# Kernel tuning notes

Measured on AMD Instinct MI355X. Metric: run time of the kernel, lower is better.

## Reference

```python
import jax, jax.numpy as jnp
import numpy as np

N_NODES = 100000
N_EDGES = 1600000
F_IN = 512
D_EMB = 128
D_HID = 64
N_CLS = 32
EPS = 1e-5


def setup_inputs() -> dict:
    key = jax.random.key(0)
    ks = jax.random.split(key, 16)
    def w(k, shape):
        fan_in = shape[0]
        return jax.random.normal(k, shape, dtype=jnp.float32) / jnp.sqrt(jnp.float32(fan_in))
    return {
        "x": jax.random.normal(ks[0], (N_NODES, F_IN), dtype=jnp.float32),
        "W1": w(ks[1], (F_IN, D_EMB)), "b1": jnp.zeros((D_EMB,), jnp.float32),
        "Wc1": w(ks[2], (D_EMB, D_HID)), "bc1": jnp.zeros((D_HID,), jnp.float32),
        "Wc2": w(ks[3], (D_HID, D_HID)), "bc2": jnp.zeros((D_HID,), jnp.float32),
        "Wc3": w(ks[4], (D_HID, D_HID)), "bc3": jnp.zeros((D_HID,), jnp.float32),
        "gamma": jnp.ones((D_HID,), jnp.float32), "beta": jnp.zeros((D_HID,), jnp.float32),
        "W2": w(ks[5], (D_HID, N_CLS)), "b2": jnp.zeros((N_CLS,), jnp.float32),
        "W3": w(ks[6], (N_CLS, N_CLS)), "b3": jnp.zeros((N_CLS,), jnp.float32),
        "edge_index": jax.random.randint(ks[7], (2, N_EDGES), 0, N_NODES, dtype=jnp.int32),
    }


def _agg_mean(h, src, dst, n):
    # gather source-node features along edges, sum into destination nodes, divide by degree
    s = jax.ops.segment_sum(h[src], dst, num_segments=n)          # [N, d]
    deg = jax.ops.segment_sum(jnp.ones((src.shape[0], 1), h.dtype), dst, num_segments=n)
    return s / jnp.maximum(deg, 1.0)


def _conv1p(h, src, dst, W, b):
    # ConvolutionalLayer_1P: neighborhood gather/aggregate -> linear -> relu
    return jax.nn.relu(_agg_mean(h, src, dst, h.shape[0]) @ W + b)


def reference(x, W1, b1, Wc1, bc1, Wc2, bc2, Wc3, bc3, gamma, beta, W2, b2, W3, b3, edge_index):
    src, dst = edge_index[0], edge_index[1]
    # linmaps1 on 0th-order ptensors == identity copy
    h = jax.nn.relu(x @ W1 + b1)                 # lin1 + relu (dropout = identity in eval)
    h = _conv1p(h, src, dst, Wc1, bc1)           # conv1
    h = _conv1p(h, src, dst, Wc2, bc2)           # conv2
    h = _conv1p(h, src, dst, Wc3, bc3)           # conv3
    mean = jnp.mean(h, axis=0)
    var = jnp.var(h, axis=0)
    h = (h - mean) * jax.lax.rsqrt(var + EPS) * gamma + beta  # batchnorm (batch stats)
    h = jax.nn.relu(h @ W2 + b2)                 # lin2 + relu (dropout = identity)
    out = h @ W3 + b3                            # lin3; linmaps0 == identity
    return out
```

## Files before the change

kernel.cpp:

```cpp
#include <hip/hip_runtime.h>
#include <cstdint>
#include <cstddef>

constexpr int F_IN  = 512;
constexpr int D_EMB = 128;
constexpr int D_HID = 64;
constexpr int N_CLS = 32;

typedef __attribute__((ext_vector_type(8))) short short8;
typedef __attribute__((ext_vector_type(4))) float floatx4;

__device__ inline unsigned short f2bf(float f) {
  union { float f; uint32_t u; } v; v.f = f;
  uint32_t r = v.u + 0x7FFF + ((v.u >> 16) & 1);
  return (unsigned short)(r >> 16);
}

__global__ __launch_bounds__(256) void wt_kernel(
    const float* __restrict__ W1, short8* __restrict__ Wt2)
{
  int idx = blockIdx.x * 256 + threadIdx.x;
  int kc8 = idx >> 10, lin = idx & 1023;
  int ct = lin >> 7, rem = lin & 127, ks = rem >> 6, ln = rem & 63;
  int col = ct * 16 + (ln & 15);
  int k0 = kc8 * 64 + ks * 32 + (ln >> 4) * 8;
  short8 s;
#pragma unroll
  for (int j = 0; j < 8; ++j)
    s[j] = (short)f2bf(W1[(size_t)(k0 + j) * D_EMB + col]);
  Wt2[idx] = s;
}

__global__ __launch_bounds__(256) void lin1_mfma_kernel(
    const float* __restrict__ X, const short8* __restrict__ Wt2,
    const float* __restrict__ b1, float* __restrict__ H1, int n)
{
  __shared__ short8 Ws[1024];
  __shared__ short8 Xs[1024];

  const int t = threadIdx.x;
  const int wave = t >> 6, lane = t & 63;
  const int quad = lane >> 4, mrow = lane & 15;
  const int node0 = blockIdx.x * 128;
  const int rloc = (wave >> 1) * 64;
  const int cw = (wave & 1) * 4;

  const float* sp[4];
  int soff[4];
#pragma unroll
  for (int i = 0; i < 4; ++i) {
    int g = t + i * 256;
    int row = g >> 3, col8 = g & 7;
    soff[i] = row * 128 + ((col8 * 16) ^ ((row & 7) << 4));
    int gr = node0 + row; if (gr >= n) gr = n - 1;
    sp[i] = &X[(size_t)gr * F_IN + col8 * 8];
  }

  floatx4 acc[4][4];
#pragma unroll
  for (int i = 0; i < 4; ++i)
#pragma unroll
    for (int j = 0; j < 4; ++j) acc[i][j] = (floatx4){0.f, 0.f, 0.f, 0.f};

  float4 xr[4][2];
  short8 wr[4];

#pragma unroll
  for (int i = 0; i < 4; ++i) {
    const float* p = sp[i];
    xr[i][0] = *(const float4*)p;
    xr[i][1] = *(const float4*)(p + 4);
    wr[i] = Wt2[t + i * 256];
  }

  for (int kc8 = 0; kc8 < 8; ++kc8) {
    short8 s8[4];
#pragma unroll
    for (int i = 0; i < 4; ++i) {
      s8[i][0] = (short)f2bf(xr[i][0].x); s8[i][1] = (short)f2bf(xr[i][0].y);
      s8[i][2] = (short)f2bf(xr[i][0].z); s8[i][3] = (short)f2bf(xr[i][0].w);
      s8[i][4] = (short)f2bf(xr[i][1].x); s8[i][5] = (short)f2bf(xr[i][1].y);
      s8[i][6] = (short)f2bf(xr[i][1].z); s8[i][7] = (short)f2bf(xr[i][1].w);
    }
    __syncthreads();
#pragma unroll
    for (int i = 0; i < 4; ++i) {
      *(short8*)((char*)Xs + soff[i]) = s8[i];
      Ws[t + i * 256] = wr[i];
    }
    __syncthreads();

    if (kc8 < 7) {
#pragma unroll
      for (int i = 0; i < 4; ++i) {
        const float* p = sp[i] + (kc8 + 1) * 64;
        xr[i][0] = *(const float4*)p;
        xr[i][1] = *(const float4*)(p + 4);
        wr[i] = Wt2[(kc8 + 1) * 1024 + t + i * 256];
      }
    }

#pragma unroll
    for (int ks = 0; ks < 2; ++ks) {
      short8 af[4], bf[4];
#pragma unroll
      for (int rt = 0; rt < 4; ++rt) {
        int row = rloc + rt * 16 + mrow;
        int byteoff = row * 128 + ((ks * 64 + quad * 16) ^ ((row & 7) << 4));
        af[rt] = *(const short8*)((const char*)Xs + byteoff);
      }
#pragma unroll
      for (int c = 0; c < 4; ++c)
        bf[c] = Ws[((cw + c) * 2 + ks) * 64 + lane];
#pragma unroll
      for (int rt = 0; rt < 4; ++rt)
#pragma unroll
        for (int c = 0; c < 4; ++c)
          acc[rt][c] = __builtin_amdgcn_mfma_f32_16x16x32_bf16(
              af[rt], bf[c], acc[rt][c], 0, 0, 0);
    }
  }

  const int rowbase = node0 + rloc;
#pragma unroll
  for (int ct = 0; ct < 4; ++ct) {
    int col = (cw + ct) * 16 + mrow;
    float bias = b1[col];
#pragma unroll
    for (int rt = 0; rt < 4; ++rt) {
#pragma unroll
      for (int r = 0; r < 4; ++r) {
        int gn = rowbase + rt * 16 + quad * 4 + r;
        if (gn < n)
          H1[(size_t)gn * D_EMB + col] = fmaxf(acc[rt][ct][r] + bias, 0.f);
      }
    }
  }
}

template<int K, bool PRE>
__global__ __launch_bounds__(256) void mm_kernel(
    const float* __restrict__ In, const int* __restrict__ deg,
    const float* __restrict__ bin, const float* __restrict__ W,
    float* __restrict__ Out, int n)
{
  __shared__ float Hs[64][K + 4];
  __shared__ float Ws[K][64];
  const int t = threadIdx.x;
  const int node0 = blockIdx.x * 64;
  constexpr int KQ = K / 4;

#pragma unroll
  for (int i = 0; i < (64 * KQ) / 256; ++i) {
    int lin = t + i * 256;
    int node = lin / KQ, kq = lin % KQ;
    int gn = node0 + node;
    float4 v = make_float4(0.f, 0.f, 0.f, 0.f);
    if (gn < n) {
      v = *(const float4*)&In[(size_t)gn * K + kq * 4];
      if (PRE) {
        float rd = 1.f / fmaxf((float)deg[gn], 1.f);
        v.x = fmaxf(v.x * rd + bin[kq * 4 + 0], 0.f);
        v.y = fmaxf(v.y * rd + bin[kq * 4 + 1], 0.f);
        v.z = fmaxf(v.z * rd + bin[kq * 4 + 2], 0.f);
        v.w = fmaxf(v.w * rd + bin[kq * 4 + 3], 0.f);
      }
    }
    *(float4*)&Hs[node][kq * 4] = v;
  }
#pragma unroll
  for (int i = 0; i < (K * 64) / 1024; ++i) {
    int lin = t + i * 256;
    ((float4*)&Ws[0][0])[lin] = ((const float4*)W)[lin];
  }
  __syncthreads();

  const int rg = t >> 4, cg = t & 15;
  float acc[4][4];
#pragma unroll
  for (int i = 0; i < 4; ++i)
#pragma unroll
    for (int j = 0; j < 4; ++j) acc[i][j] = 0.f;

#pragma unroll 8
  for (int k = 0; k < K; ++k) {
    float a[4] = {Hs[rg*4+0][k], Hs[rg*4+1][k], Hs[rg*4+2][k], Hs[rg*4+3][k]};
    float4 b = *(const float4*)&Ws[k][cg * 4];
#pragma unroll
    for (int i = 0; i < 4; ++i) {
      acc[i][0] += a[i]*b.x; acc[i][1] += a[i]*b.y;
      acc[i][2] += a[i]*b.z; acc[i][3] += a[i]*b.w;
    }
  }
#pragma unroll
  for (int i = 0; i < 4; ++i) {
    int gn = node0 + rg * 4 + i;
    if (gn < n) {
      float4 o = make_float4(acc[i][0], acc[i][1], acc[i][2], acc[i][3]);
      *(float4*)&Out[(size_t)gn * 64 + cg * 4] = o;
    }
  }
}


__global__ __launch_bounds__(256) void hist_kernel(
    const int* __restrict__ dst, int* __restrict__ G, int nE, int B, int NB)
{
  __shared__ int h[256];
  int blk = blockIdx.x, t = threadIdx.x;
  h[t] = 0;
  __syncthreads();
  int base = blk * 8192;
  int lim = min(8192, nE - base);
  for (int i = t; i < lim; i += 256)
    atomicAdd(&h[dst[base + i] >> 9], 1);
  __syncthreads();
  if (t < NB) G[t * B + blk] = h[t];
}

__global__ __launch_bounds__(256) void scan1_kernel(
    const int* __restrict__ in, int* __restrict__ out,
    int* __restrict__ bsum, int n)
{
  __shared__ int sh[256];
  int t = threadIdx.x;
  int i = blockIdx.x * 256 + t;
  int c = (i < n) ? in[i] : 0;
  sh[t] = c;
  __syncthreads();
#pragma unroll
  for (int off = 1; off < 256; off <<= 1) {
    int v = 0;
    if (t >= off) v = sh[t - off];
    __syncthreads();
    if (t >= off) sh[t] += v;
    __syncthreads();
  }
  if (i < n) out[i] = sh[t] - c;
  if (t == 255) bsum[blockIdx.x] = sh[255];
}

__global__ __launch_bounds__(256) void scan2_kernel(int* __restrict__ bsum, int nb)
{
  __shared__ int sh[256];
  __shared__ int carry;
  int t = threadIdx.x;
  if (t == 0) carry = 0;
  __syncthreads();
  for (int base = 0; base < nb; base += 256) {
    int i = base + t;
    int v = (i < nb) ? bsum[i] : 0;
    sh[t] = v;
    __syncthreads();
#pragma unroll
    for (int off = 1; off < 256; off <<= 1) {
      int u = 0;
      if (t >= off) u = sh[t - off];
      __syncthreads();
      if (t >= off) sh[t] += u;
      __syncthreads();
    }
    int c0 = carry;
    int incl = sh[t], total = sh[255];
    if (i < nb) bsum[i] = c0 + incl - v;
    __syncthreads();
    if (t == 0) carry = c0 + total;
    __syncthreads();
  }
  if (t == 0) bsum[nb] = carry;
}

__global__ __launch_bounds__(256) void scan3_kernel(
    int* __restrict__ W, const int* __restrict__ bsum, int NG, int nb)
{
  int i = blockIdx.x * 256 + threadIdx.x;
  if (i < NG) W[i] += bsum[i >> 8];
  else if (i == NG) W[NG] = bsum[nb];
}

__global__ __launch_bounds__(256) void scatter2_kernel(
    const int* __restrict__ src, const int* __restrict__ dst,
    const int* __restrict__ W, int2* __restrict__ EP, int nE, int B, int NB)
{
  __shared__ int cur[256];
  int blk = blockIdx.x, t = threadIdx.x;
  if (t < NB) cur[t] = W[t * B + blk];
  __syncthreads();
  int base = blk * 8192;
  int lim = min(8192, nE - base);
  for (int i = t; i < lim; i += 256) {
    int s = src[base + i], d = dst[base + i];
    int slot = atomicAdd(&cur[d >> 9], 1);
    EP[slot] = make_int2(s, d);
  }
}

__global__ __launch_bounds__(256) void fillc_kernel(
    const int2* __restrict__ EP, const int* __restrict__ W,
    int* __restrict__ cnt, int* __restrict__ offs, int* __restrict__ adj,
    int n, int nE, int B, int NB)
{
  __shared__ int h[512];
  int b = blockIdx.x, t = threadIdx.x;
  int segStart = W[b * B];
  int segEnd = (b == NB - 1) ? nE : W[(b + 1) * B];
  int nodeBase = b << 9;

  h[t] = 0; h[t + 256] = 0;
  __syncthreads();
  for (int i = segStart + t; i < segEnd; i += 256)
    atomicAdd(&h[EP[i].y - nodeBase], 1);
  __syncthreads();
  int c0 = h[t], c1 = h[t + 256];
#pragma unroll
  for (int off = 1; off < 512; off <<= 1) {
    int a = (t >= off) ? h[t - off] : 0;
    int bb = (t + 256 >= off) ? h[t + 256 - off] : 0;
    __syncthreads();
    h[t] += a; h[t + 256] += bb;
    __syncthreads();
  }
  int e0 = h[t] - c0, e1 = h[t + 256] - c1;
  int g0 = nodeBase + t, g1 = nodeBase + t + 256;
  if (g0 < n) { cnt[g0] = c0; offs[g0] = segStart + e0; }
  if (g1 < n) { cnt[g1] = c1; offs[g1] = segStart + e1; }
  if (b == 0 && t == 0) offs[n] = nE;
  __syncthreads();
  h[t] = e0; h[t + 256] = e1;
  __syncthreads();
  for (int i = segStart + t; i < segEnd; i += 256) {
    int2 p = EP[i];
    int slot = atomicAdd(&h[p.y - nodeBase], 1);
    adj[segStart + slot] = p.x;
  }
}

__global__ __launch_bounds__(256) void gather_kernel(
    const float* __restrict__ P, const int* __restrict__ offs,
    const int* __restrict__ adj, float* __restrict__ A, int n)
{
  int node = (blockIdx.x * 256 + threadIdx.x) >> 6;
  int lane = threadIdx.x & 63;
  if (node >= n) return;
  int beg = offs[node], end = offs[node + 1];
  float acc0 = 0.f, acc1 = 0.f;
  int j = beg;
  while (j < end) {
    int m = min(end - j, 64);
    int idx = (lane < m) ? adj[j + lane] : 0;
    int q = 0;
    for (; q + 1 < m; q += 2) {
      int s0 = __shfl(idx, q, 64);
      int s1 = __shfl(idx, q + 1, 64);
      acc0 += P[(size_t)s0 * 64 + lane];
      acc1 += P[(size_t)s1 * 64 + lane];
    }
    if (q < m) {
      int s0 = __shfl(idx, q, 64);
      acc0 += P[(size_t)s0 * 64 + lane];
    }
    j += m;
  }
  A[(size_t)node * 64 + lane] = acc0 + acc1;
}

__global__ __launch_bounds__(256) void post3_kernel(
    const float* __restrict__ A, const int* __restrict__ deg,
    const float* __restrict__ bc3, float* __restrict__ H4,
    float* __restrict__ stats, int n)
{
  int t = threadIdx.x;
  int f = t & 63, q = t >> 6;
  float b = bc3[f];
  float s = 0.f, s2 = 0.f;
  for (int node = blockIdx.x * 4 + q; node < n; node += gridDim.x * 4) {
    float v = fmaxf(A[(size_t)node * 64 + f] / fmaxf((float)deg[node], 1.f) + b, 0.f);
    H4[(size_t)node * 64 + f] = v;
    s += v; s2 += v * v;
  }
  __shared__ float red[2][4][64];
  red[0][q][f] = s; red[1][q][f] = s2;
  __syncthreads();
  if (t < 128) {
    int which = t >> 6, ff = t & 63;
    float a = red[which][0][ff] + red[which][1][ff] +
              red[which][2][ff] + red[which][3][ff];
    atomicAdd(&stats[which * 64 + ff], a);
  }
}

__global__ __launch_bounds__(256) void fold_kernel(
    const float* __restrict__ stats, const float* __restrict__ gamma,
    const float* __restrict__ beta, const float* __restrict__ W2,
    const float* __restrict__ b2, float* __restrict__ W2f,
    float* __restrict__ b2f, int n)
{
  __shared__ float rsg[64], corr[64];
  int t = threadIdx.x;
  if (t < 64) {
    float m = stats[t] / (float)n;
    float var = stats[64 + t] / (float)n - m * m;
    float rs = rsqrtf(var + 1e-5f);
    float g = gamma[t] * rs;
    rsg[t] = g;
    corr[t] = beta[t] - m * g;
  }
  __syncthreads();
#pragma unroll
  for (int i = 0; i < 8; ++i) {
    int lin = t + i * 256;
    int k = lin >> 5;
    W2f[lin] = rsg[k] * W2[lin];
  }
  if (t < 32) {
    float a = b2[t];
    for (int k = 0; k < 64; ++k) a += corr[k] * W2[k * 32 + t];
    b2f[t] = a;
  }
}

__global__ __launch_bounds__(256) void final_kernel(
    const float* __restrict__ H4, const float* __restrict__ W2f,
    const float* __restrict__ b2f, const float* __restrict__ W3,
    const float* __restrict__ b3, float* __restrict__ Out, int n)
{
  __shared__ float Hs[64][68];
  __shared__ float W2s[64][32];
  __shared__ float W3s[32][32];
  __shared__ float Us[64][36];
  __shared__ float b2s[32], b3s[32];
  const int t = threadIdx.x;
  const int node0 = blockIdx.x * 64;

#pragma unroll
  for (int i = 0; i < 4; ++i) {
    int lin = t + i * 256;
    int node = lin >> 4, kq = lin & 15;
    float4 v = make_float4(0.f, 0.f, 0.f, 0.f);
    if (node0 + node < n)
      v = *(const float4*)&H4[(size_t)(node0 + node) * 64 + kq * 4];
    *(float4*)&Hs[node][kq * 4] = v;
  }
#pragma unroll
  for (int i = 0; i < 2; ++i) {
    int lin = t + i * 256;
    ((float4*)&W2s[0][0])[lin] = ((const float4*)W2f)[lin];
  }
  ((float4*)&W3s[0][0])[t & 255] = ((const float4*)W3)[t & 255];
  if (t < 32) { b2s[t] = b2f[t]; b3s[t] = b3[t]; }
  __syncthreads();

  const int rg = t >> 4, cg = t & 15;
  float acc[4][2] = {{0.f,0.f},{0.f,0.f},{0.f,0.f},{0.f,0.f}};
#pragma unroll 8
  for (int k = 0; k < 64; ++k) {
    float a[4] = {Hs[rg*4+0][k], Hs[rg*4+1][k], Hs[rg*4+2][k], Hs[rg*4+3][k]};
    float w0 = W2s[k][cg*2], w1 = W2s[k][cg*2+1];
#pragma unroll
    for (int i = 0; i < 4; ++i) { acc[i][0] += a[i]*w0; acc[i][1] += a[i]*w1; }
  }
#pragma unroll
  for (int i = 0; i < 4; ++i) {
    Us[rg*4+i][cg*2+0] = fmaxf(acc[i][0] + b2s[cg*2+0], 0.f);
    Us[rg*4+i][cg*2+1] = fmaxf(acc[i][1] + b2s[cg*2+1], 0.f);
  }
  __syncthreads();

  float acc2[4][2] = {{0.f,0.f},{0.f,0.f},{0.f,0.f},{0.f,0.f}};
#pragma unroll
  for (int k = 0; k < 32; ++k) {
    float a[4] = {Us[rg*4+0][k], Us[rg*4+1][k], Us[rg*4+2][k], Us[rg*4+3][k]};
    float w0 = W3s[k][cg*2], w1 = W3s[k][cg*2+1];
#pragma unroll
    for (int i = 0; i < 4; ++i) { acc2[i][0] += a[i]*w0; acc2[i][1] += a[i]*w1; }
  }
  float (*Os)[36] = (float(*)[36])Hs;
#pragma unroll
  for (int i = 0; i < 4; ++i) {
    Os[rg*4+i][cg*2+0] = acc2[i][0] + b3s[cg*2+0];
    Os[rg*4+i][cg*2+1] = acc2[i][1] + b3s[cg*2+1];
  }
  __syncthreads();
#pragma unroll
  for (int i = 0; i < 2; ++i) {
    int lin = t + i * 256;
    int node = lin >> 3, c4 = lin & 7;
    if (node0 + node < n)
      *(float4*)&Out[(size_t)(node0 + node) * 32 + c4 * 4] =
          *(float4*)&Os[node][c4 * 4];
  }
}

extern "C" void kernel_launch(void* const* d_in, const int* in_sizes, int n_in,
                              void* d_out, int out_size, void* d_ws, size_t ws_size,
                              hipStream_t stream)
{
  const float* X     = (const float*)d_in[0];
  const float* W1    = (const float*)d_in[1];
  const float* b1    = (const float*)d_in[2];
  const float* Wc1   = (const float*)d_in[3];
  const float* bc1   = (const float*)d_in[4];
  const float* Wc2   = (const float*)d_in[5];
  const float* bc2   = (const float*)d_in[6];
  const float* Wc3   = (const float*)d_in[7];
  const float* bc3   = (const float*)d_in[8];
  const float* gamma = (const float*)d_in[9];
  const float* beta  = (const float*)d_in[10];
  const float* W2    = (const float*)d_in[11];
  const float* b2    = (const float*)d_in[12];
  const float* W3    = (const float*)d_in[13];
  const float* b3    = (const float*)d_in[14];
  const int*   ei    = (const int*)d_in[15];

  const int n  = in_sizes[0] / F_IN;
  const int nE = in_sizes[15] / 2;
  const int* src  = ei;
  const int* dstv = ei + nE;

  const int NB = (n + 511) >> 9;
  const int B  = (nE + 8191) >> 13;
  const int NG = NB * B;
  const int nbG = (NG + 255) / 256;

  float* ws    = (float*)d_ws;
  float* H1    = ws;
  float* P     = H1 + (size_t)n * D_EMB;
  float* A     = P  + (size_t)n * D_HID;
  float* stats = A  + (size_t)n * D_HID;
  float* W2f   = stats + 128;
  float* b2f   = W2f + 2048;
  int*   cnt   = (int*)(b2f + 32);
  int*   offs  = cnt + n;
  int*   G     = offs + n + 1;
  int*   W     = G + NG;
  int*   bsum  = W + NG + 1;
  int*   adj   = bsum + nbG + 1;
  uintptr_t epAddr = ((uintptr_t)(adj + nE) + 7) & ~(uintptr_t)7;
  int2*  EP    = (int2*)epAddr;
  short8* Wt2  = (short8*)(EP + nE);
  float* H4    = H1;

  const int nb  = (n + 63) / 64;
  const int gatherBlocks = (int)(((long long)n * 64 + 255) / 256);

  hipMemsetAsync(stats, 0, 128 * sizeof(float), stream);

  wt_kernel<<<32, 256, 0, stream>>>(W1, Wt2);
  lin1_mfma_kernel<<<(n + 127) / 128, 256, 0, stream>>>(X, Wt2, b1, H1, n);

  hist_kernel<<<B, 256, 0, stream>>>(dstv, G, nE, B, NB);
  scan1_kernel<<<nbG, 256, 0, stream>>>(G, W, bsum, NG);
  scan2_kernel<<<1, 256, 0, stream>>>(bsum, nbG);
  scan3_kernel<<<(NG + 256) / 256, 256, 0, stream>>>(W, bsum, NG, nbG);
  scatter2_kernel<<<B, 256, 0, stream>>>(src, dstv, W, EP, nE, B, NB);
  fillc_kernel<<<NB, 256, 0, stream>>>(EP, W, cnt, offs, adj, n, nE, B, NB);

  mm_kernel<128, false><<<nb, 256, 0, stream>>>(H1, nullptr, nullptr, Wc1, P, n);
  gather_kernel<<<gatherBlocks, 256, 0, stream>>>(P, offs, adj, A, n);

  mm_kernel<64, true><<<nb, 256, 0, stream>>>(A, cnt, bc1, Wc2, P, n);
  gather_kernel<<<gatherBlocks, 256, 0, stream>>>(P, offs, adj, A, n);

  mm_kernel<64, true><<<nb, 256, 0, stream>>>(A, cnt, bc2, Wc3, P, n);
  gather_kernel<<<gatherBlocks, 256, 0, stream>>>(P, offs, adj, A, n);

  post3_kernel<<<256, 256, 0, stream>>>(A, cnt, bc3, H4, stats, n);

  fold_kernel<<<1, 256, 0, stream>>>(stats, gamma, beta, W2, b2, W2f, b2f, n);
  final_kernel<<<nb, 256, 0, stream>>>(H4, W2f, b2f, W3, b3, (float*)d_out, n);
}
```

Baseline: 730.1 us.

## Fuse neighbor gather with next-layer matmul and BN stats; drop scan3 and memset

Each neighbor gather is merged into the following 64x64 matmul (gmm_kernel), so the aggregated features sit in shared memory and are never written out and re-read. The last gather is merged with the bias/relu/batch-stat step (gp_kernel). The scan3 pass is folded into scatter2 and fillc, which now add the block sums inline, and zeroing of the stats buffer moves into hist_kernel in place of the memset. Ping-pong buffers replace the separate A buffer. The fused blocks process 8 nodes per wave serially, which can lower the memory-level parallelism of the gather compared with one node per wave.

Result: faster. 692.4 us (-5.2%).

```diff
diff --git a/kernel.cpp b/kernel.cpp
--- a/kernel.cpp
+++ b/kernel.cpp
@@ -138,10 +138,9 @@
   }
 }
 
-template<int K, bool PRE>
+template<int K>
 __global__ __launch_bounds__(256) void mm_kernel(
-    const float* __restrict__ In, const int* __restrict__ deg,
-    const float* __restrict__ bin, const float* __restrict__ W,
+    const float* __restrict__ In, const float* __restrict__ W,
     float* __restrict__ Out, int n)
 {
   __shared__ float Hs[64][K + 4];
@@ -156,16 +155,8 @@
     int node = lin / KQ, kq = lin % KQ;
     int gn = node0 + node;
     float4 v = make_float4(0.f, 0.f, 0.f, 0.f);
-    if (gn < n) {
+    if (gn < n)
       v = *(const float4*)&In[(size_t)gn * K + kq * 4];
-      if (PRE) {
-        float rd = 1.f / fmaxf((float)deg[gn], 1.f);
-        v.x = fmaxf(v.x * rd + bin[kq * 4 + 0], 0.f);
-        v.y = fmaxf(v.y * rd + bin[kq * 4 + 1], 0.f);
-        v.z = fmaxf(v.z * rd + bin[kq * 4 + 2], 0.f);
-        v.w = fmaxf(v.w * rd + bin[kq * 4 + 3], 0.f);
-      }
-    }
     *(float4*)&Hs[node][kq * 4] = v;
   }
 #pragma unroll
@@ -202,12 +193,149 @@
   }
 }
 
+__global__ __launch_bounds__(512) void gmm_kernel(
+    const float* __restrict__ P, const int* __restrict__ offs,
+    const int* __restrict__ adj, const int* __restrict__ deg,
+    const float* __restrict__ bin, const float* __restrict__ W,
+    float* __restrict__ Out, int n)
+{
+  __shared__ float Hs[64][68];
+  __shared__ float Ws[64][64];
+  const int t = threadIdx.x;
+  const int wave = t >> 6, lane = t & 63;
+  const int node0 = blockIdx.x * 64;
+
+#pragma unroll
+  for (int i = 0; i < 2; ++i) {
+    int lin = t + i * 512;
+    ((float4*)&Ws[0][0])[lin] = ((const float4*)W)[lin];
+  }
+  const float bb = bin[lane];
+
+#pragma unroll 1
+  for (int nd = 0; nd < 8; ++nd) {
+    int ln = wave * 8 + nd;
+    int node = node0 + ln;
+    float v = 0.f;
+    if (node < n) {
+      int beg = offs[node], end = offs[node + 1];
+      float a0 = 0.f, a1 = 0.f, a2 = 0.f, a3 = 0.f;
+      int j = beg;
+      while (j < end) {
+        int m = min(end - j, 64);
+        int idx = (lane < m) ? adj[j + lane] : 0;
+        int q = 0;
+        for (; q + 3 < m; q += 4) {
+          int s0 = __shfl(idx, q, 64),     s1 = __shfl(idx, q + 1, 64);
+          int s2 = __shfl(idx, q + 2, 64), s3 = __shfl(idx, q + 3, 64);
+          a0 += P[(size_t)s0 * 64 + lane];
+          a1 += P[(size_t)s1 * 64 + lane];
+          a2 += P[(size_t)s2 * 64 + lane];
+          a3 += P[(size_t)s3 * 64 + lane];
+        }
+        for (; q < m; ++q) {
+          int s0 = __shfl(idx, q, 64);
+          a0 += P[(size_t)s0 * 64 + lane];
+        }
+        j += m;
+      }
+      float rd = 1.f / fmaxf((float)deg[node], 1.f);
+      v = fmaxf(((a0 + a2) + (a1 + a3)) * rd + bb, 0.f);
+    }
+    Hs[ln][lane] = v;
+  }
+  __syncthreads();
+
+  const int rg = t >> 4, cg = t & 15;
+  float acc[2][4];
+#pragma unroll
+  for (int i = 0; i < 2; ++i)
+#pragma unroll
+    for (int j = 0; j < 4; ++j) acc[i][j] = 0.f;
+
+#pragma unroll 8
+  for (int k = 0; k < 64; ++k) {
+    float a[2] = {Hs[rg * 2 + 0][k], Hs[rg * 2 + 1][k]};
+    float4 b = *(const float4*)&Ws[k][cg * 4];
+#pragma unroll
+    for (int i = 0; i < 2; ++i) {
+      acc[i][0] += a[i]*b.x; acc[i][1] += a[i]*b.y;
+      acc[i][2] += a[i]*b.z; acc[i][3] += a[i]*b.w;
+    }
+  }
+#pragma unroll
+  for (int i = 0; i < 2; ++i) {
+    int gn = node0 + rg * 2 + i;
+    if (gn < n) {
+      float4 o = make_float4(acc[i][0], acc[i][1], acc[i][2], acc[i][3]);
+      *(float4*)&Out[(size_t)gn * 64 + cg * 4] = o;
+    }
+  }
+}
+
+__global__ __launch_bounds__(512) void gp_kernel(
+    const float* __restrict__ P, const int* __restrict__ offs,
+    const int* __restrict__ adj, const int* __restrict__ deg,
+    const float* __restrict__ bc3, float* __restrict__ H4,
+    float* __restrict__ stats, int n)
+{
+  const int t = threadIdx.x;
+  const int wave = t >> 6, lane = t & 63;
+  const int node0 = blockIdx.x * 64;
+  const float bb = bc3[lane];
+  float s = 0.f, s2 = 0.f;
+
+#pragma unroll 1
+  for (int nd = 0; nd < 8; ++nd) {
+    int node = node0 + wave * 8 + nd;
+    if (node >= n) break;
+    int beg = offs[node], end = offs[node + 1];
+    float a0 = 0.f, a1 = 0.f, a2 = 0.f, a3 = 0.f;
+    int j = beg;
+    while (j < end) {
+      int m = min(end - j, 64);
+      int idx = (lane < m) ? adj[j + lane] : 0;
+      int q = 0;
+      for (; q + 3 < m; q += 4) {
+        int s0 = __shfl(idx, q, 64),     s1 = __shfl(idx, q + 1, 64);
+        int s2i = __shfl(idx, q + 2, 64), s3 = __shfl(idx, q + 3, 64);
+        a0 += P[(size_t)s0 * 64 + lane];
+        a1 += P[(size_t)s1 * 64 + lane];
+        a2 += P[(size_t)s2i * 64 + lane];
+        a3 += P[(size_t)s3 * 64 + lane];
+      }
+      for (; q < m; ++q) {
+        int s0 = __shfl(idx, q, 64);
+        a0 += P[(size_t)s0 * 64 + lane];
+      }
+      j += m;
+    }
+    float rd = 1.f / fmaxf((float)deg[node], 1.f);
+    float v = fmaxf(((a0 + a2) + (a1 + a3)) * rd + bb, 0.f);
+    H4[(size_t)node * 64 + lane] = v;
+    s += v; s2 += v * v;
+  }
+
+  __shared__ float red[2][8][64];
+  red[0][wave][lane] = s; red[1][wave][lane] = s2;
+  __syncthreads();
+  if (t < 128) {
+    int which = t >> 6, ff = t & 63;
+    float a = 0.f;
+#pragma unroll
+    for (int w = 0; w < 8; ++w) a += red[which][w][ff];
+    atomicAdd(&stats[which * 64 + ff], a);
+  }
+}
+
 
 __global__ __launch_bounds__(256) void hist_kernel(
-    const int* __restrict__ dst, int* __restrict__ G, int nE, int B, int NB)
+    const int* __restrict__ dst, int* __restrict__ G,
+    float* __restrict__ stats, int nE, int B, int NB)
 {
   __shared__ int h[256];
   int blk = blockIdx.x, t = threadIdx.x;
+  if (blk == 0 && t < 128) stats[t] = 0.f;
   h[t] = 0;
   __syncthreads();
   int base = blk * 8192;
@@ -270,21 +398,17 @@
   if (t == 0) bsum[nb] = carry;
 }
 
-__global__ __launch_bounds__(256) void scan3_kernel(
-    int* __restrict__ W, const int* __restrict__ bsum, int NG, int nb)
-{
-  int i = blockIdx.x * 256 + threadIdx.x;
-  if (i < NG) W[i] += bsum[i >> 8];
-  else if (i == NG) W[NG] = bsum[nb];
-}
-
 __global__ __launch_bounds__(256) void scatter2_kernel(
     const int* __restrict__ src, const int* __restrict__ dst,
-    const int* __restrict__ W, int2* __restrict__ EP, int nE, int B, int NB)
+    const int* __restrict__ W, const int* __restrict__ bsum,
+    int2* __restrict__ EP, int nE, int B, int NB)
 {
   __shared__ int cur[256];
   int blk = blockIdx.x, t = threadIdx.x;
-  if (t < NB) cur[t] = W[t * B + blk];
+  if (t < NB) {
+    int gi = t * B + blk;
+    cur[t] = W[gi] + bsum[gi >> 8];
+  }
   __syncthreads();
   int base = blk * 8192;
   int lim = min(8192, nE - base);
@@ -297,13 +421,15 @@
 
 __global__ __launch_bounds__(256) void fillc_kernel(
     const int2* __restrict__ EP, const int* __restrict__ W,
+    const int* __restrict__ bsum,
     int* __restrict__ cnt, int* __restrict__ offs, int* __restrict__ adj,
     int n, int nE, int B, int NB)
 {
   __shared__ int h[512];
   int b = blockIdx.x, t = threadIdx.x;
-  int segStart = W[b * B];
-  int segEnd = (b == NB - 1) ? nE : W[(b + 1) * B];
+  int g0i = b * B;
+  int segStart = W[g0i] + bsum[g0i >> 8];
+  int segEnd = (b == NB - 1) ? nE : (W[g0i + B] + bsum[(g0i + B) >> 8]);
   int nodeBase = b << 9;
 
   h[t] = 0; h[t + 256] = 0;
@@ -332,60 +458,6 @@
     int2 p = EP[i];
     int slot = atomicAdd(&h[p.y - nodeBase], 1);
     adj[segStart + slot] = p.x;
-  }
-}
-
-__global__ __launch_bounds__(256) void gather_kernel(
-    const float* __restrict__ P, const int* __restrict__ offs,
-    const int* __restrict__ adj, float* __restrict__ A, int n)
-{
-  int node = (blockIdx.x * 256 + threadIdx.x) >> 6;
-  int lane = threadIdx.x & 63;
-  if (node >= n) return;
-  int beg = offs[node], end = offs[node + 1];
-  float acc0 = 0.f, acc1 = 0.f;
-  int j = beg;
-  while (j < end) {
-    int m = min(end - j, 64);
-    int idx = (lane < m) ? adj[j + lane] : 0;
-    int q = 0;
-    for (; q + 1 < m; q += 2) {
-      int s0 = __shfl(idx, q, 64);
-      int s1 = __shfl(idx, q + 1, 64);
-      acc0 += P[(size_t)s0 * 64 + lane];
-      acc1 += P[(size_t)s1 * 64 + lane];
-    }
-    if (q < m) {
-      int s0 = __shfl(idx, q, 64);
-      acc0 += P[(size_t)s0 * 64 + lane];
-    }
-    j += m;
-  }
-  A[(size_t)node * 64 + lane] = acc0 + acc1;
-}
-
-__global__ __launch_bounds__(256) void post3_kernel(
-    const float* __restrict__ A, const int* __restrict__ deg,
-    const float* __restrict__ bc3, float* __restrict__ H4,
-    float* __restrict__ stats, int n)
-{
-  int t = threadIdx.x;
-  int f = t & 63, q = t >> 6;
-  float b = bc3[f];
-  float s = 0.f, s2 = 0.f;
-  for (int node = blockIdx.x * 4 + q; node < n; node += gridDim.x * 4) {
-    float v = fmaxf(A[(size_t)node * 64 + f] / fmaxf((float)deg[node], 1.f) + b, 0.f);
-    H4[(size_t)node * 64 + f] = v;
-    s += v; s2 += v * v;
-  }
-  __shared__ float red[2][4][64];
-  red[0][q][f] = s; red[1][q][f] = s2;
-  __syncthreads();
-  if (t < 128) {
-    int which = t >> 6, ff = t & 63;
-    float a = red[which][0][ff] + red[which][1][ff] +
-              red[which][2][ff] + red[which][3][ff];
-    atomicAdd(&stats[which * 64 + ff], a);
   }
 }
 
@@ -524,9 +596,9 @@
 
   float* ws    = (float*)d_ws;
   float* H1    = ws;
-  float* P     = H1 + (size_t)n * D_EMB;
-  float* A     = P  + (size_t)n * D_HID;
-  float* stats = A  + (size_t)n * D_HID;
+  float* Pa    = H1 + (size_t)n * D_EMB;
+  float* Pb    = Pa + (size_t)n * D_HID;
+  float* stats = Pb + (size_t)n * D_HID;
   float* W2f   = stats + 128;
   float* b2f   = W2f + 2048;
   int*   cnt   = (int*)(b2f + 32);
@@ -541,30 +613,23 @@
   float* H4    = H1;
 
   const int nb  = (n + 63) / 64;
-  const int gatherBlocks = (int)(((long long)n * 64 + 255) / 256);
-
-  hipMemsetAsync(stats, 0, 128 * sizeof(float), stream);
 
   wt_kernel<<<32, 256, 0, stream>>>(W1, Wt2);
   lin1_mfma_kernel<<<(n + 127) / 128, 256, 0, stream>>>(X, Wt2, b1, H1, n);
 
-  hist_kernel<<<B, 256, 0, stream>>>(dstv, G, nE, B, NB);
+  hist_kernel<<<B, 256, 0, stream>>>(dstv, G, stats, nE, B, NB);
   scan1_kernel<<<nbG, 256, 0, stream>>>(G, W, bsum, NG);
   scan2_kernel<<<1, 256, 0, stream>>>(bsum, nbG);
-  scan3_kernel<<<(NG + 256) / 256, 256, 0, stream>>>(W, bsum, NG, nbG);
-  scatter2_kernel<<<B, 256, 0, stream>>>(src, dstv, W, EP, nE, B, NB);
-  fillc_kernel<<<NB, 256, 0, stream>>>(EP, W, cnt, offs, adj, n, nE, B, NB);
-
-  mm_kernel<128, false><<<nb, 256, 0, stream>>>(H1, nullptr, nullptr, Wc1, P, n);
-  gather_kernel<<<gatherBlocks, 256, 0, stream>>>(P, offs, adj, A, n);
-
-  mm_kernel<64, true><<<nb, 256, 0, stream>>>(A, cnt, bc1, Wc2, P, n);
-  gather_kernel<<<gatherBlocks, 256, 0, stream>>>(P, offs, adj, A, n);
-
-  mm_kernel<64, true><<<nb, 256, 0, stream>>>(A, cnt, bc2, Wc3, P, n);
-  gather_kernel<<<gatherBlocks, 256, 0, stream>>>(P, offs, adj, A, n);
-
-  post3_kernel<<<256, 256, 0, stream>>>(A, cnt, bc3, H4, stats, n);
+  scatter2_kernel<<<B, 256, 0, stream>>>(src, dstv, W, bsum, EP, nE, B, NB);
+  fillc_kernel<<<NB, 256, 0, stream>>>(EP, W, bsum, cnt, offs, adj, n, nE, B, NB);
+
+  mm_kernel<128><<<nb, 256, 0, stream>>>(H1, Wc1, Pa, n);
+
+  gmm_kernel<<<nb, 512, 0, stream>>>(Pa, offs, adj, cnt, bc1, Wc2, Pb, n);
+
+  gmm_kernel<<<nb, 512, 0, stream>>>(Pb, offs, adj, cnt, bc2, Wc3, Pa, n);
+
+  gp_kernel<<<nb, 512, 0, stream>>>(Pa, offs, adj, cnt, bc3, H4, stats, n);
 
   fold_kernel<<<1, 256, 0, stream>>>(stats, gamma, beta, W2, b2, W2f, b2f, n);
   final_kernel<<<nb, 256, 0, stream>>>(H4, W2f, b2f, W3, b3, (float*)d_out, n);
```
